# Optimization experiments

Measured on AMD Instinct MI355X. Metric: run time of the kernel, lower is better.

## Reference

```python
import jax, jax.numpy as jnp
import numpy as np

VOCAB, EMB, FEAT = 30000, 300, 2048
B, NQ, NW, NK = 256, 32, 12, 64


def setup_inputs() -> dict:
    key = jax.random.key(0)
    ks = jax.random.split(key, 10)
    return {
        "wv": jax.random.normal(ks[0], (VOCAB, EMB), jnp.float32),
        "Wf": jax.random.normal(ks[1], (EMB, FEAT), jnp.float32) * 0.02,
        "bf": jax.random.normal(ks[2], (EMB,), jnp.float32) * 0.02,
        "Wp": jax.random.normal(ks[3], (EMB, EMB), jnp.float32) * 0.05,
        "bp": jax.random.normal(ks[4], (EMB,), jnp.float32) * 0.02,
        "Wm": jax.random.normal(ks[5], (EMB, EMB), jnp.float32) * 0.05,
        "bm": jax.random.normal(ks[6], (EMB,), jnp.float32) * 0.02,
        "feature": jax.random.normal(ks[7], (B, NK, FEAT), jnp.float32),
        "query": jax.random.randint(ks[8], (B, NQ, NW), 0, VOCAB),
        "label": jax.random.randint(ks[9], (B, NK), 0, VOCAB),
    }


def reference(wv, Wf, bf, Wp, bp, Wm, bm, feature, query, label):
    # Dropouts act as identity in eval mode.
    eps = 1e-5
    q_emb = wv[query]                                   # [B, queries, words, D]
    k_emb = wv[label] + feature @ Wf.T + bf             # [B, objects, D]
    scale = 1.0 / np.sqrt(EMB)
    att = jnp.einsum('byqd,bkd->byqk', q_emb, k_emb) * scale
    att = jax.nn.softmax(att, axis=-1)                  # over objects
    q_max_att = jnp.max(att, axis=3)                    # [B, queries, words]
    neg_inf = -jnp.finfo(q_max_att.dtype).max
    q_max_att = jnp.where(query == 0, neg_inf, q_max_att)
    q_max_norm_att = jax.nn.softmax(q_max_att, axis=-1) / 5.0
    p_emb = jnp.einsum('byq,byqd->byd', q_max_norm_att, q_emb)  # [B, queries, D]
    p_emb = (p_emb @ Wp.T + bp) + eps * (p_emb @ Wm.T + bm)
    return p_emb, k_emb
```

## Files before the change

### kernel.cpp

```cpp
#include <hip/hip_runtime.h>

typedef unsigned short u16;
typedef unsigned int u32;
typedef __bf16 bf16x8 __attribute__((ext_vector_type(8)));
typedef float f32x4 __attribute__((ext_vector_type(4)));

#if defined(__has_builtin)
#  if __has_builtin(__builtin_amdgcn_cvt_pk_bf16_f32)
#    define PK_BF16 1
#  endif
#endif

__device__ __forceinline__ u16 f2bu(float f){
  u32 u = __float_as_uint(f);
  return (u16)((u + 0x7fffu + ((u >> 16) & 1u)) >> 16);
}
__device__ __forceinline__ float b2f(u16 u){
  union { float f; u32 i; } v; v.i = ((u32)u) << 16; return v.f;
}
__device__ __forceinline__ u32 pkbf(float a, float b){
#ifdef PK_BF16
  typedef __bf16 bf16x2 __attribute__((ext_vector_type(2)));
  union { bf16x2 h; u32 u; } c;
  c.h = __builtin_amdgcn_cvt_pk_bf16_f32(a, b);
  return c.u;
#else
  return (u32)f2bu(a) | ((u32)f2bu(b) << 16);
#endif
}
__device__ __forceinline__ void glds16(const u16* g, u16* l){
  __builtin_amdgcn_global_load_lds(
      (const __attribute__((address_space(1))) void*)g,
      (__attribute__((address_space(3))) void*)l, 16, 0, 0);
}
__device__ __forceinline__ void glds16f(const float* g, float* l){
  __builtin_amdgcn_global_load_lds(
      (const __attribute__((address_space(1))) void*)g,
      (__attribute__((address_space(3))) void*)l, 16, 0, 0);
}

__global__ __launch_bounds__(256) void prep_wc(
    const float* __restrict__ Wp, const float* __restrict__ bp,
    const float* __restrict__ Wm, const float* __restrict__ bm,
    u16* __restrict__ Wc, float* __restrict__ bc)
{
  int idx = blockIdx.x * 256 + threadIdx.x;
  if (idx < 384 * 160) {
    int n = idx / 160, k = (idx % 160) * 2;
    float v0 = 0.f, v1 = 0.f;
    if (n < 300 && k < 300) {
      v0 = Wp[n * 300 + k]     + 1e-5f * Wm[n * 300 + k];
      v1 = Wp[n * 300 + k + 1] + 1e-5f * Wm[n * 300 + k + 1];
    }
    ((u32*)Wc)[idx] = pkbf(v0, v1);
    if (idx < 384) bc[idx] = (idx < 300) ? bp[idx] + 1e-5f * bm[idx] : 0.f;
  }
}

__global__ __launch_bounds__(256) void prep_wv16(
    const float* __restrict__ wv, u16* __restrict__ wv16)
{
  int idx = blockIdx.x * 256 + threadIdx.x;
  if (idx < 30000 * 160) {
    int row = idx / 160, k = (idx % 160) * 2;
    float v0 = 0.f, v1 = 0.f;
    if (k < 300) {
      v0 = wv[(size_t)row * 300 + k];
      v1 = wv[(size_t)row * 300 + k + 1];
    }
    ((u32*)wv16)[idx] = pkbf(v0, v1);
  }
}

__global__ __launch_bounds__(256) void prep_wf16(
    const float* __restrict__ Wf, u16* __restrict__ Wf16)
{
  int i = blockIdx.x * 256 + threadIdx.x;
  if (i < 384 * 1024) {
    int row = i >> 10, c2 = (i & 1023) * 2;
    float v0 = 0.f, v1 = 0.f;
    if (row < 300) {
      v0 = Wf[(size_t)row * 2048 + c2];
      v1 = Wf[(size_t)row * 2048 + c2 + 1];
    }
    ((u32*)Wf16)[i] = pkbf(v0, v1);
  }
}

template <int GLDS>
__global__ __launch_bounds__(256) void gemm0_kernel(
    const float* __restrict__ A, const float* __restrict__ B,
    const u16* __restrict__ Af16, const u16* __restrict__ Bf16,
    const float* __restrict__ bias,
    const int* __restrict__ label, const float* __restrict__ wv,
    float* __restrict__ C, u16* __restrict__ kemb16)
{
  __shared__ __align__(16) u16 As[128 * 32];
  __shared__ __align__(16) u16 Bs[128 * 32];
  const int lda = 2048, K = 2048, nbn = 3, nsrc = 300;
  int t = threadIdx.x;
  int bm = (blockIdx.x / nbn) * 128;
  int bn = (blockIdx.x % nbn) * 128;
  int lane = t & 63, w = t >> 6;
  int wm = (w >> 1) * 64, wn = (w & 1) * 64;

  f32x4 acc[4][4];
  for (int i = 0; i < 4; i++)
    for (int j = 0; j < 4; j++)
      for (int r = 0; r < 4; r++) acc[i][j][r] = 0.f;

  int mrow = lane & 15, q = lane >> 4;

  for (int kk = 0; kk < K; kk += 32) {
    #pragma unroll
    for (int p = 0; p < 2; p++) {
      int idx = t + p * 256;
      int row = idx >> 2, ch = idx & 3;
      int brow = bn + row;
      if (brow >= nsrc) brow = 0;
      const float4* ap = (const float4*)&A[(size_t)(bm + row) * lda + kk + ch * 8];
      float4 a0 = ap[0], a1 = ap[1];
      const float4* bpp = (const float4*)&B[(size_t)brow * lda + kk + ch * 8];
      float4 b0 = bpp[0], b1 = bpp[1];
      union { u32 u[4]; uint4 v; } pa, pb;
      pa.u[0] = pkbf(a0.x, a0.y); pa.u[1] = pkbf(a0.z, a0.w);
      pa.u[2] = pkbf(a1.x, a1.y); pa.u[3] = pkbf(a1.z, a1.w);
      pb.u[0] = pkbf(b0.x, b0.y); pb.u[1] = pkbf(b0.z, b0.w);
      pb.u[2] = pkbf(b1.x, b1.y); pb.u[3] = pkbf(b1.z, b1.w);
      *(uint4*)&As[idx * 8] = pa.v;
      *(uint4*)&Bs[idx * 8] = pb.v;
    }
    __syncthreads();

    bf16x8 af[4], bfr[4];
    #pragma unroll
    for (int i = 0; i < 4; i++)
      af[i] = *(const bf16x8*)&As[(wm + i * 16 + mrow) * 32 + q * 8];
    #pragma unroll
    for (int j = 0; j < 4; j++)
      bfr[j] = *(const bf16x8*)&Bs[(wn + j * 16 + mrow) * 32 + q * 8];
    #pragma unroll
    for (int i = 0; i < 4; i++)
      #pragma unroll
      for (int j = 0; j < 4; j++)
        acc[i][j] = __builtin_amdgcn_mfma_f32_16x16x32_bf16(
            af[i], bfr[j], acc[i][j], 0, 0, 0);
    __syncthreads();
  }

  #pragma unroll
  for (int i = 0; i < 4; i++)
    #pragma unroll
    for (int j = 0; j < 4; j++) {
      int col = bn + wn + j * 16 + (lane & 15);
      int rb = bm + wm + i * 16 + (lane >> 4) * 4;
      #pragma unroll
      for (int r = 0; r < 4; r++) {
        int m = rb + r;
        if (col < 300) {
          float v = acc[i][j][r];
          v += bias[col] + wv[(size_t)label[m] * 300 + col];
          C[(size_t)m * 300 + col] = v;
          if (kemb16) kemb16[(size_t)m * 320 + col] = f2bu(v);
        } else if (kemb16 && col < 320) {
          kemb16[(size_t)m * 320 + col] = 0;
        }
      }
    }
}

__global__ __launch_bounds__(256) void gemm0v3_kernel(
    const float* __restrict__ A, const u16* __restrict__ Bf16,
    const float* __restrict__ bias, const int* __restrict__ label,
    const float* __restrict__ wv, float* __restrict__ C,
    u16* __restrict__ kemb16)
{
  __shared__ __align__(16) float As[2][64 * 32];
  __shared__ __align__(16) u16  Bs[2][128 * 32];
  const int NIT = 64;
  int t = threadIdx.x;
  int g = blockIdx.x;
  int seq = (g & 7) * 96 + (g >> 3);
  int bm = (seq / 3) * 64;
  int bn = (seq % 3) * 128;
  int lane = t & 63, w = t >> 6;
  int wm = (w >> 1) * 32, wn = (w & 1) * 64;

  f32x4 acc[2][4];
  #pragma unroll
  for (int i = 0; i < 2; i++)
    #pragma unroll
    for (int j = 0; j < 4; j++)
      #pragma unroll
      for (int r = 0; r < 4; r++) acc[i][j][r] = 0.f;

  int mrow = lane & 15, q = lane >> 4;
  int rlA = lane >> 3, chA = lane & 7;
  int rlB = lane >> 2, chB = lane & 3;
  int csA = (chA ^ rlA) * 4;
  int csB = chB * 8;

  const float* gA0 = &A[(size_t)(bm + w * 16 + rlA) * 2048 + csA];
  const float* gA1 = &A[(size_t)(bm + w * 16 + 8 + rlA) * 2048 + csA];
  const u16*   gB0 = &Bf16[(size_t)(bn + w * 32 + rlB) * 2048 + csB];
  const u16*   gB1 = &Bf16[(size_t)(bn + w * 32 + 16 + rlB) * 2048 + csB];

  auto STAGE = [&](int buf, int kk) {
    glds16f(gA0 + kk, &As[buf][(w * 16) * 32]);
    glds16f(gA1 + kk, &As[buf][(w * 16 + 8) * 32]);
    glds16(gB0 + kk, &Bs[buf][(w * 32) * 32]);
    glds16(gB1 + kk, &Bs[buf][(w * 32 + 16) * 32]);
  };

  STAGE(0, 0);
  __syncthreads();

  for (int it = 0; it < NIT; ++it) {
    int cur = it & 1;
    if (it + 1 < NIT) STAGE(cur ^ 1, (it + 1) * 32);

    bf16x8 af[2], bfr[4];
    #pragma unroll
    for (int i = 0; i < 2; i++) {
      int r = wm + i * 16 + mrow;
      int c0 = ((q * 2) ^ (r & 7)) * 4;
      int c1 = ((q * 2 + 1) ^ (r & 7)) * 4;
      f32x4 x = *(const f32x4*)&As[cur][r * 32 + c0];
      f32x4 y = *(const f32x4*)&As[cur][r * 32 + c1];
      union { u32 u[4]; bf16x8 h; } cc;
      cc.u[0] = pkbf(x[0], x[1]); cc.u[1] = pkbf(x[2], x[3]);
      cc.u[2] = pkbf(y[0], y[1]); cc.u[3] = pkbf(y[2], y[3]);
      af[i] = cc.h;
    }
    #pragma unroll
    for (int j = 0; j < 4; j++)
      bfr[j] = *(const bf16x8*)&Bs[cur][(wn + j * 16 + mrow) * 32 + q * 8];
    #pragma unroll
    for (int i = 0; i < 2; i++)
      #pragma unroll
      for (int j = 0; j < 4; j++)
        acc[i][j] = __builtin_amdgcn_mfma_f32_16x16x32_bf16(
            af[i], bfr[j], acc[i][j], 0, 0, 0);

    __syncthreads();
  }

  #pragma unroll
  for (int i = 0; i < 2; i++)
    #pragma unroll
    for (int j = 0; j < 4; j++) {
      int col = bn + wn + j * 16 + (lane & 15);
      int rb = bm + wm + i * 16 + (lane >> 4) * 4;
      #pragma unroll
      for (int r = 0; r < 4; r++) {
        int m = rb + r;
        if (col < 300) {
          float v = acc[i][j][r] + bias[col] + wv[(size_t)label[m] * 300 + col];
          C[(size_t)m * 300 + col] = v;
          kemb16[(size_t)m * 320 + col] = f2bu(v);
        } else if (col < 320) {
          kemb16[(size_t)m * 320 + col] = 0;
        }
      }
    }
}

#define KES 344
template <int FULL>
__global__ __launch_bounds__(256) void attn_kernel(
    const float* __restrict__ wv, const u16* __restrict__ wv16,
    const int* __restrict__ query,
    const float* __restrict__ kout, const u16* __restrict__ kemb16,
    u16* __restrict__ praw)
{
  __shared__ __align__(16) u16 ke[64 * KES];
  __shared__ __align__(16) int qoff[192];
  __shared__ __align__(16) float awd[192];
  __shared__ __align__(16) float wt[192];

  int blk = blockIdx.x, b = blk >> 1, bh = blk & 1;
  int t = threadIdx.x;
  int lane = t & 63, w = t >> 6;

  if (FULL) {
    for (int i = t; i < 2560; i += 256) {
      int row = i / 40, ch = i % 40;
      *(uint4*)&ke[row * KES + ch * 8] =
          *(const uint4*)&kemb16[(size_t)(b * 64 + row) * 320 + ch * 8];
    }
  } else {
    for (int i = t; i < 4800; i += 256) {
      int row = i / 75, c4 = i % 75;
      float4 v = *(const float4*)&kout[(size_t)(b * 64 + row) * 300 + c4 * 4];
      *(u32*)&ke[row * KES + c4 * 4]     = pkbf(v.x, v.y);
      *(u32*)&ke[row * KES + c4 * 4 + 2] = pkbf(v.z, v.w);
    }
    for (int i = t; i < 640; i += 256) {
      int row = i / 10, c2 = i % 10;
      *(u32*)&ke[row * KES + 300 + c2 * 2] = 0;
    }
  }
  if (t < 192)
    qoff[t] = query[b * 384 + bh * 192 + t] * (FULL ? 320 : 300);
  __syncthreads();

  int mrow = lane & 15, q = lane >> 4;
  f32x4 acc[3][4];
  #pragma unroll
  for (int i = 0; i < 3; i++)
    #pragma unroll
    for (int j = 0; j < 4; j++)
      #pragma unroll
      for (int r = 0; r < 4; r++) acc[i][j][r] = 0.f;

  int base[3];
  #pragma unroll
  for (int i = 0; i < 3; i++) base[i] = qoff[w * 48 + i * 16 + mrow];
  int keb = mrow * KES + q * 8;

  bf16x8 afn[3];
  #pragma unroll
  for (int i = 0; i < 3; i++) {
    if (FULL)
      afn[i] = *(const bf16x8*)&wv16[(size_t)base[i] + q * 8];
  }

  for (int k0 = 0; k0 < 320; k0 += 32) {
    bf16x8 af[3], bfr[4];
    #pragma unroll
    for (int i = 0; i < 3; i++) {
      if (FULL) {
        af[i] = afn[i];
        if (k0 + 32 < 320)
          afn[i] = *(const bf16x8*)&wv16[(size_t)base[i] + k0 + 32 + q * 8];
      } else {
        int cs = k0 + q * 8;
        union { u32 u[4]; bf16x8 h; } c;
        if (cs + 8 <= 300) {
          const float4* p = (const float4*)&wv[(size_t)base[i] + cs];
          float4 x = p[0], y = p[1];
          c.u[0] = pkbf(x.x, x.y); c.u[1] = pkbf(x.z, x.w);
          c.u[2] = pkbf(y.x, y.y); c.u[3] = pkbf(y.z, y.w);
        } else if (cs < 300) {
          float4 x = *(const float4*)&wv[(size_t)base[i] + 296];
          c.u[0] = pkbf(x.x, x.y); c.u[1] = pkbf(x.z, x.w);
          c.u[2] = 0; c.u[3] = 0;
        } else {
          c.u[0] = 0; c.u[1] = 0; c.u[2] = 0; c.u[3] = 0;
        }
        af[i] = c.h;
      }
    }
    #pragma unroll
    for (int j = 0; j < 4; j++)
      bfr[j] = *(const bf16x8*)&ke[j * 16 * KES + keb + k0];
    #pragma unroll
    for (int i = 0; i < 3; i++)
      #pragma unroll
      for (int j = 0; j < 4; j++)
        acc[i][j] = __builtin_amdgcn_mfma_f32_16x16x32_bf16(
            af[i], bfr[j], acc[i][j], 0, 0, 0);
  }

  const float scale = 0.05773502691896258f;
  #pragma unroll
  for (int i = 0; i < 3; i++)
    #pragma unroll
    for (int r = 0; r < 4; r++) {
      float mx = fmaxf(fmaxf(acc[i][0][r], acc[i][1][r]),
                       fmaxf(acc[i][2][r], acc[i][3][r]));
      #pragma unroll
      for (int d = 1; d < 16; d <<= 1)
        mx = fmaxf(mx, __shfl_xor(mx, d));
      float se = 0.f;
      #pragma unroll
      for (int j = 0; j < 4; j++)
        se += __expf((acc[i][j][r] - mx) * scale);
      #pragma unroll
      for (int d = 1; d < 16; d <<= 1)
        se += __shfl_xor(se, d);
      if (mrow == 0) {
        int wl = w * 48 + i * 16 + q * 4 + r;
        awd[wl] = (qoff[wl] == 0) ? -3.402823466e38f : (1.0f / se);
      }
    }
  __syncthreads();

  if (t < 16) {
    int yb = t * 12;
    float m2 = -3.402823466e38f;
    for (int i = 0; i < 12; i++) m2 = fmaxf(m2, awd[yb + i]);
    float e[12], s2 = 0.f;
    for (int i = 0; i < 12; i++) { e[i] = __expf(awd[yb + i] - m2); s2 += e[i]; }
    float inv = 0.2f / s2;
    for (int i = 0; i < 12; i++) wt[yb + i] = e[i] * inv;
  }
  __syncthreads();

  #pragma unroll
  for (int yy = 0; yy < 4; yy++) {
    int yl = w * 4 + yy;
    int row = b * 32 + bh * 16 + yl;
    if (FULL) {
      if (lane < 40) {
        float s[8];
        #pragma unroll
        for (int e = 0; e < 8; e++) s[e] = 0.f;
        for (int i = 0; i < 12; i++) {
          float g = wt[yl * 12 + i];
          union { uint4 v; u16 h[8]; } qv;
          qv.v = *(const uint4*)&wv16[(size_t)qoff[yl * 12 + i] + lane * 8];
          #pragma unroll
          for (int e = 0; e < 8; e++) s[e] += g * b2f(qv.h[e]);
        }
        union { uint4 v; u16 h[8]; } o;
        #pragma unroll
        for (int e = 0; e < 8; e++) o.h[e] = f2bu(s[e]);
        *(uint4*)&praw[(size_t)row * 320 + lane * 8] = o.v;
      }
    } else {
      #pragma unroll
      for (int c = 0; c < 5; c++) {
        int d = c * 64 + lane;
        float s = 0.f;
        if (d < 300)
          for (int i = 0; i < 12; i++)
            s += wt[yl * 12 + i] * wv[(size_t)qoff[yl * 12 + i] + d];
        praw[(size_t)row * 320 + d] = f2bu(s);
      }
    }
  }
}

__global__ __launch_bounds__(256) void proj_kernel(
    const u16* __restrict__ praw, const u16* __restrict__ Wc,
    const float* __restrict__ bc, float* __restrict__ P)
{
  __shared__ __align__(16) u16 As[128 * 32];
  __shared__ __align__(16) u16 Bs[128 * 32];
  int t = threadIdx.x;
  int bm = (blockIdx.x / 3) * 128;
  int bn = (blockIdx.x % 3) * 128;
  int lane = t & 63, w = t >> 6;
  int wm = (w >> 1) * 64, wn = (w & 1) * 64;

  f32x4 acc[4][4];
  for (int i = 0; i < 4; i++)
    for (int j = 0; j < 4; j++)
      for (int r = 0; r < 4; r++) acc[i][j][r] = 0.f;

  int mrow = lane & 15, q = lane >> 4;

  for (int kk = 0; kk < 320; kk += 32) {
    int r0 = w * 32;
    int rl = lane >> 2, ch = lane & 3;
    #pragma unroll
    for (int p = 0; p < 2; p++) {
      int row = r0 + p * 16 + rl;
      glds16(&praw[(size_t)(bm + row) * 320 + kk + ch * 8],
             &As[(r0 + p * 16) * 32]);
      glds16(&Wc[(size_t)(bn + row) * 320 + kk + ch * 8],
             &Bs[(r0 + p * 16) * 32]);
    }
    __syncthreads();

    bf16x8 af[4], bfr[4];
    #pragma unroll
    for (int i = 0; i < 4; i++)
      af[i] = *(const bf16x8*)&As[(wm + i * 16 + mrow) * 32 + q * 8];
    #pragma unroll
    for (int j = 0; j < 4; j++)
      bfr[j] = *(const bf16x8*)&Bs[(wn + j * 16 + mrow) * 32 + q * 8];
    #pragma unroll
    for (int i = 0; i < 4; i++)
      #pragma unroll
      for (int j = 0; j < 4; j++)
        acc[i][j] = __builtin_amdgcn_mfma_f32_16x16x32_bf16(
            af[i], bfr[j], acc[i][j], 0, 0, 0);
    __syncthreads();
  }

  #pragma unroll
  for (int i = 0; i < 4; i++)
    #pragma unroll
    for (int j = 0; j < 4; j++) {
      int col = bn + wn + j * 16 + (lane & 15);
      if (col >= 300) continue;
      int rb = bm + wm + i * 16 + (lane >> 4) * 4;
      #pragma unroll
      for (int r = 0; r < 4; r++)
        P[(size_t)(rb + r) * 300 + col] = acc[i][j][r] + bc[col];
    }
}

extern "C" void kernel_launch(void* const* d_in, const int* in_sizes, int n_in,
                              void* d_out, int out_size, void* d_ws,
                              size_t ws_size, hipStream_t stream)
{
  const float* wv      = (const float*)d_in[0];
  const float* Wf      = (const float*)d_in[1];
  const float* bf      = (const float*)d_in[2];
  const float* Wp      = (const float*)d_in[3];
  const float* bp      = (const float*)d_in[4];
  const float* Wm      = (const float*)d_in[5];
  const float* bm      = (const float*)d_in[6];
  const float* feature = (const float*)d_in[7];
  const int*   query   = (const int*)d_in[8];
  const int*   label   = (const int*)d_in[9];

  float* out   = (float*)d_out;
  float* p_out = out;
  float* k_out = out + 2457600;

  char* ws = (char*)d_ws;
  int t2 = ws_size >= (size_t)103857664;
  int t1 = ws_size >= (size_t)35175936;
  u16 *wf16 = 0, *wv16 = 0, *kemb16 = 0, *praw, *Wc;
  float* bc;
  if (t2) {
    wv16   = (u16*)(ws + 67108864);
    kemb16 = (u16*)(ws + 86308864);
    praw   = (u16*)(ws + 96794624);
    Wc     = (u16*)(ws + 102037504);
    wf16   = (u16*)(ws + 102283264);
    bc     = (float*)(ws + 103856128);
  } else if (t1) {
    wv16   = (u16*)ws;
    kemb16 = (u16*)(ws + 19200000);
    praw   = (u16*)(ws + 29685760);
    Wc     = (u16*)(ws + 34928640);
    bc     = (float*)(ws + 35174400);
  } else {
    praw   = (u16*)ws;
    Wc     = (u16*)(ws + 5242880);
    bc     = (float*)(ws + 5488640);
  }

  prep_wc<<<240, 256, 0, stream>>>(Wp, bp, Wm, bm, Wc, bc);
  if (t1 || t2)
    prep_wv16<<<18750, 256, 0, stream>>>(wv, wv16);
  if (t2) {
    prep_wf16<<<1536, 256, 0, stream>>>(Wf, wf16);
    gemm0v3_kernel<<<768, 256, 0, stream>>>(feature, wf16, bf,
                                            label, wv, k_out, kemb16);
  } else {
    gemm0_kernel<0><<<384, 256, 0, stream>>>(feature, Wf, 0, 0, bf,
                                             label, wv, k_out, kemb16);
  }

  if (t1 || t2)
    attn_kernel<1><<<512, 256, 0, stream>>>(wv, wv16, query, k_out,
                                            kemb16, praw);
  else
    attn_kernel<0><<<512, 256, 0, stream>>>(wv, wv16, query, k_out,
                                            kemb16, praw);

  proj_kernel<<<192, 256, 0, stream>>>(praw, Wc, bc, p_out);
}
```

Measured before the change: 353.0 us.

## Retile feature GEMM into single-wave 64x64 blocks without barriers

The feature projection GEMM moves from 256-thread blocks with 64x128 tiles to 64-thread single-wave blocks with 64x64 tiles. This cuts the padded N dimension from 384 to 320 columns, so less wasted MFMA work is done. Because each block is a single wave, block barriers are replaced by explicit vmcnt waits on the double-buffered async LDS loads. The trade-off is that the fp32 feature matrix is now re-read five times per row block instead of three, and there are more, smaller blocks with higher per-thread register use.

```diff
diff --git a/kernel.cpp b/kernel.cpp
--- a/kernel.cpp
+++ b/kernel.cpp
@@ -169,62 +169,62 @@
     }
 }
 
-__global__ __launch_bounds__(256) void gemm0v3_kernel(
+__global__ __launch_bounds__(64) void gemm0v5_kernel(
     const float* __restrict__ A, const u16* __restrict__ Bf16,
     const float* __restrict__ bias, const int* __restrict__ label,
     const float* __restrict__ wv, float* __restrict__ C,
     u16* __restrict__ kemb16)
 {
   __shared__ __align__(16) float As[2][64 * 32];
-  __shared__ __align__(16) u16  Bs[2][128 * 32];
-  const int NIT = 64;
-  int t = threadIdx.x;
+  __shared__ __align__(16) u16  Bs[2][64 * 32];
+  int lane = threadIdx.x;
   int g = blockIdx.x;
-  int seq = (g & 7) * 96 + (g >> 3);
-  int bm = (seq / 3) * 64;
-  int bn = (seq % 3) * 128;
-  int lane = t & 63, w = t >> 6;
-  int wm = (w >> 1) * 32, wn = (w & 1) * 64;
-
-  f32x4 acc[2][4];
-  #pragma unroll
-  for (int i = 0; i < 2; i++)
+  int xcd = g & 7, loc = g >> 3;
+  int mloc = loc / 5, nn = loc % 5;
+  int bm = (xcd * 32 + mloc) * 64;
+  int bn = nn * 64;
+  int mrow = lane & 15, q = lane >> 4;
+
+  f32x4 acc[4][4];
+  #pragma unroll
+  for (int i = 0; i < 4; i++)
     #pragma unroll
     for (int j = 0; j < 4; j++)
       #pragma unroll
       for (int r = 0; r < 4; r++) acc[i][j][r] = 0.f;
 
-  int mrow = lane & 15, q = lane >> 4;
   int rlA = lane >> 3, chA = lane & 7;
   int rlB = lane >> 2, chB = lane & 3;
-  int csA = (chA ^ rlA) * 4;
-  int csB = chB * 8;
-
-  const float* gA0 = &A[(size_t)(bm + w * 16 + rlA) * 2048 + csA];
-  const float* gA1 = &A[(size_t)(bm + w * 16 + 8 + rlA) * 2048 + csA];
-  const u16*   gB0 = &Bf16[(size_t)(bn + w * 32 + rlB) * 2048 + csB];
-  const u16*   gB1 = &Bf16[(size_t)(bn + w * 32 + 16 + rlB) * 2048 + csB];
-
-  auto STAGE = [&](int buf, int kk) {
-    glds16f(gA0 + kk, &As[buf][(w * 16) * 32]);
-    glds16f(gA1 + kk, &As[buf][(w * 16 + 8) * 32]);
-    glds16(gB0 + kk, &Bs[buf][(w * 32) * 32]);
-    glds16(gB1 + kk, &Bs[buf][(w * 32 + 16) * 32]);
-  };
-
-  STAGE(0, 0);
-  __syncthreads();
-
-  for (int it = 0; it < NIT; ++it) {
+  const float* gA = &A[(size_t)(bm + rlA) * 2048 + ((chA ^ rlA) << 2)];
+  const u16*   gB = &Bf16[(size_t)(bn + rlB) * 2048 + (chB << 3)];
+
+#define STAGE_V5(buf, kk) do {                                          \
+    _Pragma("unroll")                                                   \
+    for (int p = 0; p < 8; p++)                                         \
+      glds16f(gA + (size_t)p * 8 * 2048 + (kk), &As[buf][(p * 8) * 32]);\
+    _Pragma("unroll")                                                   \
+    for (int p = 0; p < 4; p++)                                         \
+      glds16(gB + (size_t)p * 16 * 2048 + (kk), &Bs[buf][(p * 16) * 32]);\
+  } while (0)
+
+  STAGE_V5(0, 0);
+
+  for (int it = 0; it < 64; ++it) {
     int cur = it & 1;
-    if (it + 1 < NIT) STAGE(cur ^ 1, (it + 1) * 32);
-
-    bf16x8 af[2], bfr[4];
-    #pragma unroll
-    for (int i = 0; i < 2; i++) {
-      int r = wm + i * 16 + mrow;
-      int c0 = ((q * 2) ^ (r & 7)) * 4;
-      int c1 = ((q * 2 + 1) ^ (r & 7)) * 4;
+    if (it < 63) {
+      STAGE_V5(cur ^ 1, (it + 1) * 32);
+      asm volatile("s_waitcnt vmcnt(12)" ::: "memory");
+    } else {
+      asm volatile("s_waitcnt vmcnt(0)" ::: "memory");
+    }
+    __builtin_amdgcn_sched_barrier(0);
+
+    bf16x8 af[4], bfr[4];
+    #pragma unroll
+    for (int i = 0; i < 4; i++) {
+      int r = i * 16 + mrow;
+      int c0 = ((2 * q) ^ (r & 7)) * 4;
+      int c1 = ((2 * q + 1) ^ (r & 7)) * 4;
       f32x4 x = *(const f32x4*)&As[cur][r * 32 + c0];
       f32x4 y = *(const f32x4*)&As[cur][r * 32 + c1];
       union { u32 u[4]; bf16x8 h; } cc;
@@ -234,23 +234,22 @@
     }
     #pragma unroll
     for (int j = 0; j < 4; j++)
-      bfr[j] = *(const bf16x8*)&Bs[cur][(wn + j * 16 + mrow) * 32 + q * 8];
-    #pragma unroll
-    for (int i = 0; i < 2; i++)
+      bfr[j] = *(const bf16x8*)&Bs[cur][(j * 16 + mrow) * 32 + q * 8];
+    #pragma unroll
+    for (int i = 0; i < 4; i++)
       #pragma unroll
       for (int j = 0; j < 4; j++)
         acc[i][j] = __builtin_amdgcn_mfma_f32_16x16x32_bf16(
             af[i], bfr[j], acc[i][j], 0, 0, 0);
-
-    __syncthreads();
-  }
-
-  #pragma unroll
-  for (int i = 0; i < 2; i++)
+  }
+#undef STAGE_V5
+
+  #pragma unroll
+  for (int i = 0; i < 4; i++)
     #pragma unroll
     for (int j = 0; j < 4; j++) {
-      int col = bn + wn + j * 16 + (lane & 15);
-      int rb = bm + wm + i * 16 + (lane >> 4) * 4;
+      int col = bn + j * 16 + (lane & 15);
+      int rb = bm + i * 16 + (lane >> 4) * 4;
       #pragma unroll
       for (int r = 0; r < 4; r++) {
         int m = rb + r;
@@ -258,7 +257,7 @@
           float v = acc[i][j][r] + bias[col] + wv[(size_t)label[m] * 300 + col];
           C[(size_t)m * 300 + col] = v;
           kemb16[(size_t)m * 320 + col] = f2bu(v);
-        } else if (col < 320) {
+        } else {
           kemb16[(size_t)m * 320 + col] = 0;
         }
       }
@@ -541,7 +540,7 @@
     prep_wv16<<<18750, 256, 0, stream>>>(wv, wv16);
   if (t2) {
     prep_wf16<<<1536, 256, 0, stream>>>(Wf, wf16);
-    gemm0v3_kernel<<<768, 256, 0, stream>>>(feature, wf16, bf,
+    gemm0v5_kernel<<<1280, 64, 0, stream>>>(feature, wf16, bf,
                                             label, wv, k_out, kemb16);
   } else {
     gemm0_kernel<0><<<384, 256, 0, stream>>>(feature, Wf, 0, 0, bf,
```

New measurement: 366.9 us. 1.04x slower.
